# Performance work log

Hardware: AMD Instinct MI355X
Metric: run time of the kernel (lower is better)

## Reference

```python
import jax, jax.numpy as jnp
import numpy as np

IN_DIM = 1024
HIDDEN = 1024
NUM_HEAD = 16
HEAD_DIM = HIDDEN // NUM_HEAD
B, S = 4, 2048


def setup_inputs() -> dict:
    key = jax.random.key(0)
    ks = jax.random.split(key, 10)
    sc = 1.0 / np.sqrt(IN_DIM)
    inp = {
        "x": jax.random.normal(ks[0], (B, S, IN_DIM), dtype=jnp.float32),
        "mask": jnp.ones((B, 1, 1, S), dtype=jnp.int32),
        "Wq": jax.random.normal(ks[1], (IN_DIM, HIDDEN), dtype=jnp.float32) * sc,
        "bq": jnp.zeros((HIDDEN,), dtype=jnp.float32),
        "Wk": jax.random.normal(ks[2], (IN_DIM, HIDDEN), dtype=jnp.float32) * sc,
        "bk": jnp.zeros((HIDDEN,), dtype=jnp.float32),
        "Wv": jax.random.normal(ks[3], (IN_DIM, HIDDEN), dtype=jnp.float32) * sc,
        "bv": jnp.zeros((HIDDEN,), dtype=jnp.float32),
        "Wo": jax.random.normal(ks[4], (HIDDEN, IN_DIM), dtype=jnp.float32) * sc,
        "bo": jnp.zeros((IN_DIM,), dtype=jnp.float32),
    }
    return inp


def reference(x, mask, Wq, bq, Wk, bk, Wv, bv, Wo, bo):
    Bq, Sq, _ = x.shape
    # projections -> [B, H, S, hd]
    def proj(W, b):
        return (x @ W + b).reshape(Bq, Sq, NUM_HEAD, HEAD_DIM).transpose(0, 2, 1, 3)
    q, k, v = proj(Wq, bq), proj(Wk, bk), proj(Wv, bv)
    scale = 1.0 / jnp.sqrt(jnp.asarray(HEAD_DIM, dtype=x.dtype))
    scores = jnp.einsum("bhqd,bhkd->bhqk", q, k) * scale  # [B,H,S,S]
    scores = jnp.where(mask == 0, jnp.asarray(-1e9, dtype=x.dtype), scores)
    attn = jax.nn.softmax(scores, axis=-1)
    out = jnp.einsum("bhqk,bhkd->bhqd", attn, v)  # [B,H,S,hd]
    out = out.transpose(0, 2, 1, 3).reshape(Bq, Sq, HIDDEN)
    return out @ Wo + bo
```

## Files before the change

kernel.cpp:

```cpp
#include <hip/hip_runtime.h>
#include <hip/hip_bf16.h>
#include <stdint.h>

#define BB_ 4
#define SS_ 2048
#define IND_ 1024
#define HIDD_ 1024
#define NH_ 16
#define HD_ 64

typedef __attribute__((ext_vector_type(8))) short vshort8;
typedef __attribute__((ext_vector_type(4))) short vshort4;
typedef __attribute__((ext_vector_type(4))) float vfloat4;

__device__ __forceinline__ short bf16_of(float f) {
    union { float f; uint32_t u; } v; v.f = f;
    uint32_t r = v.u + 0x7fffu + ((v.u >> 16) & 1u);
    return (short)(r >> 16);
}

__device__ __forceinline__ uint32_t pk_bf16(float lo, float hi) {
    uint32_t r;
    asm("v_cvt_pk_bf16_f32 %0, %1, %2" : "=v"(r) : "v"(lo), "v"(hi));
    return r;
}

typedef const __attribute__((address_space(1))) uint8_t* gas_ptr;
typedef __attribute__((address_space(3))) uint8_t* las_ptr;
__device__ __forceinline__ void gload16(const void* g, void* l) {
    __builtin_amdgcn_global_load_lds((gas_ptr)g, (las_ptr)l, 16, 0, 0);
}

__global__ __launch_bounds__(256) void conv_x(const float* __restrict__ x,
                                              short* __restrict__ xb, int n4) {
    int i = blockIdx.x * 256 + threadIdx.x;
    if (i >= n4) return;
    float4 v = ((const float4*)x)[i];
    vshort4 r;
    r[0] = bf16_of(v.x); r[1] = bf16_of(v.y); r[2] = bf16_of(v.z); r[3] = bf16_of(v.w);
    ((vshort4*)xb)[i] = r;
}

__global__ __launch_bounds__(256) void convT_w(const float* __restrict__ W,
                                               short* __restrict__ Wt) {
    __shared__ short tile[64][65];
    int k0 = blockIdx.x * 64, n0 = blockIdx.y * 64;
#pragma unroll
    for (int i = 0; i < 16; i++) {
        int idx = i * 256 + threadIdx.x;
        int r = idx >> 6, c = idx & 63;
        tile[c][r] = bf16_of(W[(k0 + r) * 1024 + n0 + c]);
    }
    __syncthreads();
#pragma unroll
    for (int i = 0; i < 16; i++) {
        int idx = i * 256 + threadIdx.x;
        int r = idx >> 6, c = idx & 63;
        Wt[(n0 + r) * 1024 + k0 + c] = tile[r][c];
    }
}

template <int MODE>
__global__ __launch_bounds__(256) void gemm_bf16(const short* __restrict__ A,
                                                 const short* __restrict__ Bt,
                                                 const float* __restrict__ bias,
                                                 void* __restrict__ out, float scale) {
    constexpr int Kd = 1024;
    __shared__ alignas(16) short smem[16384];
    const int t = threadIdx.x;
    const int w = t >> 6, lane = t & 63;
    const int g = lane >> 4, c = lane & 15;
    const int wm = w >> 1, wn = w & 1;
    const int m0 = blockIdx.x * 128, n0 = blockIdx.y * 128;

    const int row = t >> 2;
    const int colE = (t & 3) * 8;

    const short* ga0 = A + (size_t)(m0 + row) * Kd + colE;
    const short* ga1 = A + (size_t)(m0 + 64 + row) * Kd + colE;
    const short* gb0 = Bt + (size_t)(n0 + row) * Kd + colE;
    const short* gb1 = Bt + (size_t)(n0 + 64 + row) * Kd + colE;

    vfloat4 acc[4][4] = {};

    gload16(ga0, &smem[t * 8]);
    gload16(ga1, &smem[2048 + t * 8]);
    gload16(gb0, &smem[4096 + t * 8]);
    gload16(gb1, &smem[6144 + t * 8]);
    __syncthreads();

    for (int k0 = 0; k0 < Kd; k0 += 32) {
        const int cur = (k0 >> 5) & 1;
        const int nb = (cur ^ 1) * 8192;
        if (k0 + 32 < Kd) {
            gload16(ga0 + k0 + 32, &smem[nb + t * 8]);
            gload16(ga1 + k0 + 32, &smem[nb + 2048 + t * 8]);
            gload16(gb0 + k0 + 32, &smem[nb + 4096 + t * 8]);
            gload16(gb1 + k0 + 32, &smem[nb + 6144 + t * 8]);
        }
        const int cb = cur * 8192;
        vshort8 af[4], bfr[4];
#pragma unroll
        for (int mi = 0; mi < 4; mi++)
            af[mi] = *(const vshort8*)&smem[cb + (wm * 64 + mi * 16 + c) * 32 + g * 8];
#pragma unroll
        for (int ni = 0; ni < 4; ni++)
            bfr[ni] = *(const vshort8*)&smem[cb + 4096 + (wn * 64 + ni * 16 + c) * 32 + g * 8];
#pragma unroll
        for (int mi = 0; mi < 4; mi++)
#pragma unroll
            for (int ni = 0; ni < 4; ni++)
                acc[mi][ni] = __builtin_amdgcn_mfma_f32_16x16x32_bf16(
                    af[mi], bfr[ni], acc[mi][ni], 0, 0, 0);
        __syncthreads();
    }

#pragma unroll
    for (int ni = 0; ni < 4; ni++) {
        const int n = n0 + wn * 64 + ni * 16 + c;
        const float bv = bias[n];
#pragma unroll
        for (int mi = 0; mi < 4; mi++) {
#pragma unroll
            for (int r = 0; r < 4; r++) {
                const int m = m0 + wm * 64 + mi * 16 + g * 4 + r;
                const float v = (acc[mi][ni][r] + bv) * scale;
                if (MODE == 0) {
                    const int b = m >> 11, s = m & 2047, h = n >> 6, d = n & 63;
                    ((short*)out)[(((size_t)(b * 16 + h)) * 2048 + s) * 64 + d] = bf16_of(v);
                } else {
                    ((float*)out)[(size_t)m * 1024 + n] = v;
                }
            }
        }
    }
}

__global__ __launch_bounds__(256) void transpose_v(const short* __restrict__ V,
                                                   short* __restrict__ Vt) {
    __shared__ short tile[64][65];
    const int bh = blockIdx.y;
    const int s0 = blockIdx.x * 64;
#pragma unroll
    for (int i = 0; i < 16; i++) {
        int idx = i * 256 + threadIdx.x;
        int r = idx >> 6, c = idx & 63;
        tile[c][r] = V[((size_t)bh * 2048 + s0 + r) * 64 + c];
    }
    __syncthreads();
#pragma unroll
    for (int i = 0; i < 16; i++) {
        int idx = i * 256 + threadIdx.x;
        int r = idx >> 6, c = idx & 63;
        Vt[((size_t)bh * 64 + r) * 2048 + s0 + c] = tile[r][c];
    }
}

__device__ __forceinline__ vshort8 lds_frag(const short* base, int row, int off) {
    const int byte = row * 128 + (off ^ ((row & 7) << 4));
    return *(const vshort8*)((const char*)base + byte);
}
__device__ __forceinline__ uint2 lds_frag8B(const short* base, int row, int eoff) {
    const int byte = row * 128 + ((eoff * 2) ^ ((row & 7) << 4));
    return *(const uint2*)((const char*)base + byte);
}
__device__ __forceinline__ void lds_stg(short* base, int row, int e8, vshort8 v) {
    const int byte = row * 128 + ((e8 * 16) ^ ((row & 7) << 4));
    *(vshort8*)((char*)base + byte) = v;
}

__global__ __launch_bounds__(256) void attn_kernel(const short* __restrict__ Q,
                                                   const short* __restrict__ K,
                                                   const short* __restrict__ Vt,
                                                   const int* __restrict__ mask,
                                                   short* __restrict__ Oattn) {
    __shared__ alignas(16) short Kl[64 * 64];
    __shared__ alignas(16) short Vl[64 * 64];
    const int tid = threadIdx.x, w = tid >> 6, lane = tid & 63;
    const int g = lane >> 4, c = lane & 15;
    const int bh = blockIdx.y, bb = bh >> 4, h = bh & 15;
    const int q0 = blockIdx.x * 128 + w * 32;
    const short* Qb = Q + (size_t)bh * 2048 * 64;
    const short* Kb = K + (size_t)bh * 2048 * 64;
    const short* Vb = Vt + (size_t)bh * 64 * 2048;
    const int* mb = mask + bb * 2048;

    const int srow = tid >> 3, se8 = tid & 7;
    const int srow2 = srow + 32;

    vshort8 qa[2][2];
#pragma unroll
    for (int qt = 0; qt < 2; qt++)
#pragma unroll
        for (int kf = 0; kf < 2; kf++)
            qa[qt][kf] = *(const vshort8*)(Qb + (size_t)(q0 + qt * 16 + c) * 64 + kf * 32 + g * 8);

    vfloat4 o[2][4] = {};
    float lrunp[2] = {0.f, 0.f};

    vshort8 pk0 = *(const vshort8*)(Kb + (size_t)srow * 64 + se8 * 8);
    vshort8 pk1 = *(const vshort8*)(Kb + (size_t)srow2 * 64 + se8 * 8);
    vshort8 pv0 = *(const vshort8*)(Vb + (size_t)srow * 2048 + se8 * 8);
    vshort8 pv1 = *(const vshort8*)(Vb + (size_t)srow2 * 2048 + se8 * 8);

    for (int k0 = 0; k0 < 2048; k0 += 64) {
        __syncthreads();
        lds_stg(Kl, srow, se8, pk0);
        lds_stg(Kl, srow2, se8, pk1);
        lds_stg(Vl, srow, se8, pv0);
        lds_stg(Vl, srow2, se8, pv1);
        __syncthreads();
        if (k0 + 64 < 2048) {
            pk0 = *(const vshort8*)(Kb + (size_t)(k0 + 64 + srow) * 64 + se8 * 8);
            pk1 = *(const vshort8*)(Kb + (size_t)(k0 + 64 + srow2) * 64 + se8 * 8);
            pv0 = *(const vshort8*)(Vb + (size_t)srow * 2048 + k0 + 64 + se8 * 8);
            pv1 = *(const vshort8*)(Vb + (size_t)srow2 * 2048 + k0 + 64 + se8 * 8);
        }

        const int mv = mb[k0 + lane];
        const bool allone = __all(mv != 0);

        vshort8 kb[4][2];
#pragma unroll
        for (int kt = 0; kt < 4; kt++) {
            kb[kt][0] = lds_frag(Kl, kt * 16 + c, g * 16);
            kb[kt][1] = lds_frag(Kl, kt * 16 + c, 64 + g * 16);
        }
        vfloat4 s[2][4];
        __builtin_amdgcn_s_setprio(1);
#pragma unroll
        for (int qt = 0; qt < 2; qt++)
#pragma unroll
            for (int kt = 0; kt < 4; kt++) {
                vfloat4 z = {0.f, 0.f, 0.f, 0.f};
                z = __builtin_amdgcn_mfma_f32_16x16x32_bf16(kb[kt][0], qa[qt][0], z, 0, 0, 0);
                z = __builtin_amdgcn_mfma_f32_16x16x32_bf16(kb[kt][1], qa[qt][1], z, 0, 0, 0);
                s[qt][kt] = z;
            }
        __builtin_amdgcn_s_setprio(0);

        if (!allone) {
#pragma unroll
            for (int kt = 0; kt < 4; kt++)
#pragma unroll
                for (int r = 0; r < 4; r++) {
                    if (mb[k0 + kt * 16 + g * 4 + r] == 0) {
                        s[0][kt][r] = -3e8f;
                        s[1][kt][r] = -3e8f;
                    }
                }
        }

#pragma unroll
        for (int qt = 0; qt < 2; qt++) {
            float ps = 0.f;
#pragma unroll
            for (int kt = 0; kt < 4; kt++)
#pragma unroll
                for (int r = 0; r < 4; r++) {
                    const float p = exp2f(s[qt][kt][r]);
                    s[qt][kt][r] = p;
                    ps += p;
                }
            lrunp[qt] += ps;
        }

        __builtin_amdgcn_s_setprio(1);
#pragma unroll
        for (int u = 0; u < 2; u++) {
            union { uint32_t uu[4]; vshort8 v; } Pf[2];
#pragma unroll
            for (int qt = 0; qt < 2; qt++) {
                Pf[qt].uu[0] = pk_bf16(s[qt][2 * u][0], s[qt][2 * u][1]);
                Pf[qt].uu[1] = pk_bf16(s[qt][2 * u][2], s[qt][2 * u][3]);
                Pf[qt].uu[2] = pk_bf16(s[qt][2 * u + 1][0], s[qt][2 * u + 1][1]);
                Pf[qt].uu[3] = pk_bf16(s[qt][2 * u + 1][2], s[qt][2 * u + 1][3]);
            }
            const int e0 = (2 * u) * 16 + g * 4;
            const int e1 = (2 * u + 1) * 16 + g * 4;
#pragma unroll
            for (int dt = 0; dt < 4; dt++) {
                const uint2 x0 = lds_frag8B(Vl, dt * 16 + c, e0);
                const uint2 x1 = lds_frag8B(Vl, dt * 16 + c, e1);
                union { uint32_t uu[4]; vshort8 v; } Vf;
                Vf.uu[0] = x0.x; Vf.uu[1] = x0.y; Vf.uu[2] = x1.x; Vf.uu[3] = x1.y;
                o[0][dt] = __builtin_amdgcn_mfma_f32_16x16x32_bf16(Pf[0].v, Vf.v, o[0][dt], 0, 0, 0);
                o[1][dt] = __builtin_amdgcn_mfma_f32_16x16x32_bf16(Pf[1].v, Vf.v, o[1][dt], 0, 0, 0);
            }
        }
        __builtin_amdgcn_s_setprio(0);
    }

#pragma unroll
    for (int qt = 0; qt < 2; qt++) {
        float l = lrunp[qt];
        l += __shfl_xor(l, 16);
        l += __shfl_xor(l, 32);
#pragma unroll
        for (int r = 0; r < 4; r++) {
            const float lr = __shfl(l, (lane & 48) | (g * 4 + r));
            const float inv = 1.0f / lr;
            const int q = q0 + qt * 16 + g * 4 + r;
#pragma unroll
            for (int dt = 0; dt < 4; dt++) {
                const float v = o[qt][dt][r] * inv;
                Oattn[((size_t)bb * 2048 + q) * 1024 + h * 64 + dt * 16 + c] = bf16_of(v);
            }
        }
    }
}

extern "C" void kernel_launch(void* const* d_in, const int* in_sizes, int n_in,
                              void* d_out, int out_size, void* d_ws, size_t ws_size,
                              hipStream_t stream) {
    const float* x   = (const float*)d_in[0];
    const int*  mask = (const int*)d_in[1];
    const float* Wq  = (const float*)d_in[2];
    const float* bq  = (const float*)d_in[3];
    const float* Wk  = (const float*)d_in[4];
    const float* bk  = (const float*)d_in[5];
    const float* Wv  = (const float*)d_in[6];
    const float* bv  = (const float*)d_in[7];
    const float* Wo  = (const float*)d_in[8];
    const float* bo  = (const float*)d_in[9];
    float* out = (float*)d_out;

    short* xb  = (short*)d_ws;
    short* Wqt = xb + 8192 * 1024;
    short* Wkt = Wqt + 1024 * 1024;
    short* Wvt = Wkt + 1024 * 1024;
    short* Wot = Wvt + 1024 * 1024;
    short* Qb  = Wot + 1024 * 1024;
    short* Kb  = Qb + 8192 * 1024;
    short* Vb  = Kb + 8192 * 1024;
    short* Vtb = Vb + 8192 * 1024;
    short* att = Vtb + 8192 * 1024;

    conv_x<<<8192, 256, 0, stream>>>(x, xb, 8192 * 1024 / 4);
    dim3 gw(16, 16);
    convT_w<<<gw, 256, 0, stream>>>(Wq, Wqt);
    convT_w<<<gw, 256, 0, stream>>>(Wk, Wkt);
    convT_w<<<gw, 256, 0, stream>>>(Wv, Wvt);
    convT_w<<<gw, 256, 0, stream>>>(Wo, Wot);

    dim3 gg(64, 8);
    gemm_bf16<0><<<gg, 256, 0, stream>>>(xb, Wqt, bq, Qb, 0.125f * 1.4426950408889634f);
    gemm_bf16<0><<<gg, 256, 0, stream>>>(xb, Wkt, bk, Kb, 1.0f);
    gemm_bf16<0><<<gg, 256, 0, stream>>>(xb, Wvt, bv, Vb, 1.0f);

    transpose_v<<<dim3(32, 64), 256, 0, stream>>>(Vb, Vtb);
    attn_kernel<<<dim3(16, 64), 256, 0, stream>>>(Qb, Kb, Vtb, mask, att);

    gemm_bf16<1><<<gg, 256, 0, stream>>>(att, Wot, bo, out, 1.0f);
}
```

Baseline: 239.6 us.

## Double-buffer K/V tiles in attention and batch weight conversions into one launch

The attention kernel now keeps two LDS buffers for K and V. The next tile is written to the alternate buffer after the current tile's compute, which leaves one barrier per iteration instead of two. The four weight transpose/convert launches are merged into a single launch with a z-dimension selecting the matrix, cutting launch overhead. Doubling LDS to 32KB per block may reduce occupancy on the attention kernel.

```diff
diff --git a/kernel.cpp b/kernel.cpp
--- a/kernel.cpp
+++ b/kernel.cpp
@@ -41,8 +41,16 @@
     ((vshort4*)xb)[i] = r;
 }
 
-__global__ __launch_bounds__(256) void convT_w(const float* __restrict__ W,
-                                               short* __restrict__ Wt) {
+__global__ __launch_bounds__(256) void convT_w4(const float* __restrict__ W0,
+                                                const float* __restrict__ W1,
+                                                const float* __restrict__ W2,
+                                                const float* __restrict__ W3,
+                                                short* __restrict__ T0,
+                                                short* __restrict__ T1,
+                                                short* __restrict__ T2,
+                                                short* __restrict__ T3) {
+    const float* W = (blockIdx.z == 0) ? W0 : (blockIdx.z == 1) ? W1 : (blockIdx.z == 2) ? W2 : W3;
+    short* Wt = (blockIdx.z == 0) ? T0 : (blockIdx.z == 1) ? T1 : (blockIdx.z == 2) ? T2 : T3;
     __shared__ short tile[64][65];
     int k0 = blockIdx.x * 64, n0 = blockIdx.y * 64;
 #pragma unroll
@@ -174,8 +182,8 @@
                                                    const short* __restrict__ Vt,
                                                    const int* __restrict__ mask,
                                                    short* __restrict__ Oattn) {
-    __shared__ alignas(16) short Kl[64 * 64];
-    __shared__ alignas(16) short Vl[64 * 64];
+    __shared__ alignas(16) short Kl[2][64 * 64];
+    __shared__ alignas(16) short Vl[2][64 * 64];
     const int tid = threadIdx.x, w = tid >> 6, lane = tid & 63;
     const int g = lane >> 4, c = lane & 15;
     const int bh = blockIdx.y, bb = bh >> 4, h = bh & 15;
@@ -197,24 +205,29 @@
 
     vfloat4 o[2][4] = {};
     float lrunp[2] = {0.f, 0.f};
-
-    vshort8 pk0 = *(const vshort8*)(Kb + (size_t)srow * 64 + se8 * 8);
-    vshort8 pk1 = *(const vshort8*)(Kb + (size_t)srow2 * 64 + se8 * 8);
-    vshort8 pv0 = *(const vshort8*)(Vb + (size_t)srow * 2048 + se8 * 8);
-    vshort8 pv1 = *(const vshort8*)(Vb + (size_t)srow2 * 2048 + se8 * 8);
-
-    for (int k0 = 0; k0 < 2048; k0 += 64) {
-        __syncthreads();
-        lds_stg(Kl, srow, se8, pk0);
-        lds_stg(Kl, srow2, se8, pk1);
-        lds_stg(Vl, srow, se8, pv0);
-        lds_stg(Vl, srow2, se8, pv1);
-        __syncthreads();
-        if (k0 + 64 < 2048) {
-            pk0 = *(const vshort8*)(Kb + (size_t)(k0 + 64 + srow) * 64 + se8 * 8);
-            pk1 = *(const vshort8*)(Kb + (size_t)(k0 + 64 + srow2) * 64 + se8 * 8);
-            pv0 = *(const vshort8*)(Vb + (size_t)srow * 2048 + k0 + 64 + se8 * 8);
-            pv1 = *(const vshort8*)(Vb + (size_t)srow2 * 2048 + k0 + 64 + se8 * 8);
+    const vfloat4 ZF = {0.f, 0.f, 0.f, 0.f};
+
+    vshort8 rk0 = *(const vshort8*)(Kb + (size_t)srow * 64 + se8 * 8);
+    vshort8 rk1 = *(const vshort8*)(Kb + (size_t)srow2 * 64 + se8 * 8);
+    vshort8 rv0 = *(const vshort8*)(Vb + (size_t)srow * 2048 + se8 * 8);
+    vshort8 rv1 = *(const vshort8*)(Vb + (size_t)srow2 * 2048 + se8 * 8);
+    lds_stg(Kl[0], srow, se8, rk0);
+    lds_stg(Kl[0], srow2, se8, rk1);
+    lds_stg(Vl[0], srow, se8, rv0);
+    lds_stg(Vl[0], srow2, se8, rv1);
+    __syncthreads();
+
+    for (int t = 0; t < 32; t++) {
+        const int k0 = t * 64;
+        const short* Kc = Kl[t & 1];
+        const short* Vc = Vl[t & 1];
+        const bool more = (t + 1 < 32);
+        if (more) {
+            const int kn = k0 + 64;
+            rk0 = *(const vshort8*)(Kb + (size_t)(kn + srow) * 64 + se8 * 8);
+            rk1 = *(const vshort8*)(Kb + (size_t)(kn + srow2) * 64 + se8 * 8);
+            rv0 = *(const vshort8*)(Vb + (size_t)srow * 2048 + kn + se8 * 8);
+            rv1 = *(const vshort8*)(Vb + (size_t)srow2 * 2048 + kn + se8 * 8);
         }
 
         const int mv = mb[k0 + lane];
@@ -223,8 +236,8 @@
         vshort8 kb[4][2];
 #pragma unroll
         for (int kt = 0; kt < 4; kt++) {
-            kb[kt][0] = lds_frag(Kl, kt * 16 + c, g * 16);
-            kb[kt][1] = lds_frag(Kl, kt * 16 + c, 64 + g * 16);
+            kb[kt][0] = lds_frag(Kc, kt * 16 + c, g * 16);
+            kb[kt][1] = lds_frag(Kc, kt * 16 + c, 64 + g * 16);
         }
         vfloat4 s[2][4];
         __builtin_amdgcn_s_setprio(1);
@@ -232,10 +245,8 @@
         for (int qt = 0; qt < 2; qt++)
 #pragma unroll
             for (int kt = 0; kt < 4; kt++) {
-                vfloat4 z = {0.f, 0.f, 0.f, 0.f};
-                z = __builtin_amdgcn_mfma_f32_16x16x32_bf16(kb[kt][0], qa[qt][0], z, 0, 0, 0);
-                z = __builtin_amdgcn_mfma_f32_16x16x32_bf16(kb[kt][1], qa[qt][1], z, 0, 0, 0);
-                s[qt][kt] = z;
+                vfloat4 z = __builtin_amdgcn_mfma_f32_16x16x32_bf16(kb[kt][0], qa[qt][0], ZF, 0, 0, 0);
+                s[qt][kt] = __builtin_amdgcn_mfma_f32_16x16x32_bf16(kb[kt][1], qa[qt][1], z, 0, 0, 0);
             }
         __builtin_amdgcn_s_setprio(0);
 
@@ -280,8 +291,8 @@
             const int e1 = (2 * u + 1) * 16 + g * 4;
 #pragma unroll
             for (int dt = 0; dt < 4; dt++) {
-                const uint2 x0 = lds_frag8B(Vl, dt * 16 + c, e0);
-                const uint2 x1 = lds_frag8B(Vl, dt * 16 + c, e1);
+                const uint2 x0 = lds_frag8B(Vc, dt * 16 + c, e0);
+                const uint2 x1 = lds_frag8B(Vc, dt * 16 + c, e1);
                 union { uint32_t uu[4]; vshort8 v; } Vf;
                 Vf.uu[0] = x0.x; Vf.uu[1] = x0.y; Vf.uu[2] = x1.x; Vf.uu[3] = x1.y;
                 o[0][dt] = __builtin_amdgcn_mfma_f32_16x16x32_bf16(Pf[0].v, Vf.v, o[0][dt], 0, 0, 0);
@@ -289,6 +300,16 @@
             }
         }
         __builtin_amdgcn_s_setprio(0);
+
+        if (more) {
+            short* Kn = Kl[(t + 1) & 1];
+            short* Vn = Vl[(t + 1) & 1];
+            lds_stg(Kn, srow, se8, rk0);
+            lds_stg(Kn, srow2, se8, rk1);
+            lds_stg(Vn, srow, se8, rv0);
+            lds_stg(Vn, srow2, se8, rv1);
+            __syncthreads();
+        }
     }
 
 #pragma unroll
@@ -337,11 +358,7 @@
     short* att = Vtb + 8192 * 1024;
 
     conv_x<<<8192, 256, 0, stream>>>(x, xb, 8192 * 1024 / 4);
-    dim3 gw(16, 16);
-    convT_w<<<gw, 256, 0, stream>>>(Wq, Wqt);
-    convT_w<<<gw, 256, 0, stream>>>(Wk, Wkt);
-    convT_w<<<gw, 256, 0, stream>>>(Wv, Wvt);
-    convT_w<<<gw, 256, 0, stream>>>(Wo, Wot);
+    convT_w4<<<dim3(16, 16, 4), 256, 0, stream>>>(Wq, Wk, Wv, Wo, Wqt, Wkt, Wvt, Wot);
 
     dim3 gg(64, 8);
     gemm_bf16<0><<<gg, 256, 0, stream>>>(xb, Wqt, bq, Qb, 0.125f * 1.4426950408889634f);
```

Measured after the change: 237.2 us. Within noise of the previous version (-1.0%).
